# Kernel optimization log

Hardware: AMD Instinct MI355X
Metric: run time of the kernel (lower is better)

The kernel has to match this reference:

```python
import jax, jax.numpy as jnp
import numpy as np

C = 512
GROUPS = 16
EPS = 1e-6


def group_norm(x, gamma, beta):
    # x: (b, c, h, w)
    b, c, h, w = x.shape
    xg = x.reshape(b, GROUPS, c // GROUPS, h, w)
    mean = xg.mean(axis=(2, 3, 4), keepdims=True)
    var = xg.var(axis=(2, 3, 4), keepdims=True)
    xn = ((xg - mean) * jax.lax.rsqrt(var + EPS)).reshape(b, c, h, w)
    return xn * gamma[None, :, None, None] + beta[None, :, None, None]


def setup_inputs() -> dict:
    key = jax.random.key(0)
    ks = jax.random.split(key, 9)
    scale = 1.0 / np.sqrt(C)
    x = jax.random.normal(ks[0], (32, C, 32, 32), dtype=jnp.float32)
    return {
        "x": x,
        "gn_gamma": jnp.ones((C,), jnp.float32),
        "gn_beta": jnp.zeros((C,), jnp.float32),
        "wq": jax.random.normal(ks[1], (C, C), jnp.float32) * scale,
        "bq": jnp.zeros((C,), jnp.float32),
        "wk": jax.random.normal(ks[2], (C, C), jnp.float32) * scale,
        "bk": jnp.zeros((C,), jnp.float32),
        "wv": jax.random.normal(ks[3], (C, C), jnp.float32) * scale,
        "bv": jnp.zeros((C,), jnp.float32),
        "wp": jax.random.normal(ks[4], (C, C), jnp.float32) * scale,
        "bp": jnp.zeros((C,), jnp.float32),
    }


def reference(x, gn_gamma, gn_beta, wq, bq, wk, bk, wv, bv, wp, bp):
    b, c, h, w = x.shape
    hn = group_norm(x, gn_gamma, gn_beta).reshape(b, c, h * w)  # (b, c, n)
    # 1x1 convs == per-token channel GEMMs
    q = jnp.einsum('oc,bcn->bon', wq, hn) + bq[None, :, None]
    k = jnp.einsum('oc,bcn->bon', wk, hn) + bk[None, :, None]
    v = jnp.einsum('oc,bcn->bon', wv, hn) + bv[None, :, None]
    # scores: (b, n, m) = q^T k, scaled
    s = jnp.einsum('bcn,bcm->bnm', q, k) * (float(c) ** -0.5)
    # original subtracts the global max (shift-invariant) then softmax over dim 2
    s = s - jnp.max(s)
    attn = jax.nn.softmax(s, axis=2)
    # h_ = v @ attn^T  -> (b, c, n)
    out = jnp.einsum('bcm,bnm->bcn', v, attn)
    out = jnp.einsum('oc,bcn->bon', wp, out) + bp[None, :, None]
    return x + out.reshape(b, c, h, w)
```

## Files before the change

kernel.cpp:

```cpp
#include <hip/hip_runtime.h>
#include <hip/hip_bf16.h>

typedef unsigned short u16;
typedef __attribute__((ext_vector_type(8))) short bf16x8;
typedef __attribute__((ext_vector_type(4))) float f32x4;

__device__ __forceinline__ u16 f2bf(float f) {
  union { float f; unsigned u; } a; a.f = f;
  unsigned r = a.u + 0x7fffu + ((a.u >> 16) & 1u);
  return (u16)(r >> 16);
}

__device__ __forceinline__ u16 f2h(float f) {
  union { _Float16 h; u16 u; } c; c.h = (_Float16)f; return c.u;
}

__device__ __forceinline__ void stage_ht(const u16* __restrict__ g, int ldg,
                                         u16* __restrict__ s, int tid) {
  int lane = tid & 63, wave = tid >> 6;
#pragma unroll
  for (int t = 0; t < 2; ++t) {
    int cbase = t * 512 + wave * 64;
    int c = cbase + lane;
    int row = c >> 3;
    int q = (c & 7) ^ (row & 7);
    __builtin_amdgcn_global_load_lds(
        (const __attribute__((address_space(1))) unsigned int*)(g + (long)row * ldg + (q << 3)),
        (__attribute__((address_space(3))) unsigned int*)(s + cbase * 8),
        16, 0, 0);
  }
}

__device__ __forceinline__ void ld_a(const u16* __restrict__ Ah, int mh,
                                     int lrow, int quad, int sw, bf16x8 (&a)[4][2]) {
#pragma unroll
  for (int i = 0; i < 4; ++i) {
    int rb = (mh * 64 + i * 16 + lrow) * 64;
#pragma unroll
    for (int ks = 0; ks < 2; ++ks)
      a[i][ks] = *(const bf16x8*)&Ah[rb + (((ks * 4 + quad) ^ sw) << 3)];
  }
}

__device__ __forceinline__ void ld_b(const u16* __restrict__ Bh, int wn1, int nh,
                                     int lrow, int quad, int sw, bf16x8 (&bq)[2][2]) {
#pragma unroll
  for (int j = 0; j < 2; ++j) {
    int rb = (wn1 * 64 + (nh * 2 + j) * 16 + lrow) * 64;
#pragma unroll
    for (int ks = 0; ks < 2; ++ks)
      bq[j][ks] = *(const bf16x8*)&Bh[rb + (((ks * 4 + quad) ^ sw) << 3)];
  }
}

template <int MH, int NH>
__device__ __forceinline__ void mfma_q(bf16x8 (&a)[4][2], bf16x8 (&bq)[2][2],
                                       f32x4 (&acc)[8][4]) {
#pragma unroll
  for (int i = 0; i < 4; ++i)
#pragma unroll
    for (int j = 0; j < 2; ++j) {
      f32x4 c = acc[MH * 4 + i][NH * 2 + j];
      c = __builtin_amdgcn_mfma_f32_16x16x32_bf16(a[i][0], bq[j][0], c, 0, 0, 0);
      c = __builtin_amdgcn_mfma_f32_16x16x32_bf16(a[i][1], bq[j][1], c, 0, 0, 0);
      acc[MH * 4 + i][NH * 2 + j] = c;
    }
}

__device__ __forceinline__ void gemm256_core(
    const u16* __restrict__ Ab, const u16* __restrict__ Bb,
    int lda, int ldb, int K, int tid,
    u16* __restrict__ As, u16* __restrict__ Bs, f32x4 (&acc)[8][4]) {
  int wave = tid >> 6, lane = tid & 63;
  int wm = wave >> 2, wn = wave & 3, wn1 = wn & 1;
  int lrow = lane & 15, quad = lane >> 4;
  int sw = lrow & 7;
#pragma unroll
  for (int i = 0; i < 8; ++i)
#pragma unroll
    for (int j = 0; j < 4; ++j) acc[i][j] = (f32x4){0.f, 0.f, 0.f, 0.f};
  int nkt = K >> 6;
  stage_ht(Ab, lda, As, tid);
  stage_ht(Ab + 128L * lda, lda, As + 8192, tid);
  stage_ht(Bb, ldb, Bs, tid);
  stage_ht(Bb + 128L * ldb, ldb, Bs + 8192, tid);
  for (int kt = 0; kt < nkt; ++kt) {
    __syncthreads();
    const u16* Ah = As + ((kt & 1) * 2 + wm) * 8192;
    const u16* Bh = Bs + ((kt & 1) * 2 + (wn >> 1)) * 8192;
    bf16x8 a0[4][2], a1[4][2], bq0[2][2], bq1[2][2];
    ld_a(Ah, 0, lrow, quad, sw, a0);
    ld_b(Bh, wn1, 0, lrow, quad, sw, bq0);
    if (kt + 1 < nkt) {
      long ko = (long)(kt + 1) * 64;
      int nb = ((kt & 1) ^ 1) * 2;
      stage_ht(Ab + ko, lda, As + nb * 8192, tid);
      stage_ht(Ab + 128L * lda + ko, lda, As + (nb + 1) * 8192, tid);
      stage_ht(Bb + ko, ldb, Bs + nb * 8192, tid);
      stage_ht(Bb + 128L * ldb + ko, ldb, Bs + (nb + 1) * 8192, tid);
    }
    ld_b(Bh, wn1, 1, lrow, quad, sw, bq1);
    ld_a(Ah, 1, lrow, quad, sw, a1);
    __builtin_amdgcn_s_setprio(1);
    mfma_q<0, 0>(a0, bq0, acc);
    mfma_q<0, 1>(a0, bq1, acc);
    mfma_q<1, 1>(a1, bq1, acc);
    mfma_q<1, 0>(a1, bq0, acc);
    __builtin_amdgcn_s_setprio(0);
  }
}

__device__ __forceinline__ void epi_trans_bf16(
    f32x4 (&acc)[8][4], u16* __restrict__ C, long cbase, int m0, int n0, int ldc,
    const float* __restrict__ bias, float scale, int wm, int wn, int lrow, int quad) {
#pragma unroll
  for (int mf = 0; mf < 8; ++mf) {
    int rowbase = m0 + wm * 128 + mf * 16 + quad * 4;
    float4 b4 = bias ? *(const float4*)&bias[rowbase] : make_float4(0.f, 0.f, 0.f, 0.f);
#pragma unroll
    for (int nf = 0; nf < 4; ++nf) {
      int col = n0 + wn * 64 + nf * 16 + lrow;
      f32x4 a = acc[mf][nf];
      uint2 o;
      o.x = (unsigned)f2bf(a[0] * scale + b4.x) | ((unsigned)f2bf(a[1] * scale + b4.y) << 16);
      o.y = (unsigned)f2bf(a[2] * scale + b4.z) | ((unsigned)f2bf(a[3] * scale + b4.w) << 16);
      *(uint2*)(C + cbase + (long)col * ldc + rowbase) = o;
    }
  }
}

template <int MODE>
__global__ __launch_bounds__(512, 2) void gemm_kernel(
    const u16* __restrict__ Ag, const u16* __restrict__ Bg,
    void* __restrict__ C0, void* __restrict__ C1, void* __restrict__ C2,
    const float* __restrict__ bias0, const float* __restrict__ bias1,
    const float* __restrict__ bias2, const float* __restrict__ resid,
    int lda, int ldb, int ldc,
    long strideA, long strideB, long strideC, int K, float scale) {
  extern __shared__ u16 smem[];
  u16* As = smem;
  u16* Bs = smem + 32768;
  int tid = threadIdx.x;
  int b = blockIdx.z;
  int m0 = blockIdx.y * 256, n0 = blockIdx.x * 256;
  const u16* Ab = Ag + (long)b * strideA + (long)m0 * lda;
  const u16* Bb = Bg + (long)b * strideB + (long)n0 * ldb;
  f32x4 acc[8][4];
  gemm256_core(Ab, Bb, lda, ldb, K, tid, As, Bs, acc);

  int wave = tid >> 6, lane = tid & 63;
  int wm = wave >> 2, wn = wave & 3;
  int lrow = lane & 15, quad = lane >> 4;
  long cbase = (long)b * strideC;

  if (MODE == 0) {
    epi_trans_bf16(acc, (u16*)C0, cbase, m0, n0, ldc, bias0, scale, wm, wn, lrow, quad);
  } else if (MODE == 1) {
#pragma unroll
    for (int mf = 0; mf < 8; ++mf)
#pragma unroll
      for (int r = 0; r < 4; ++r) {
        int row = m0 + wm * 128 + mf * 16 + quad * 4 + r;
#pragma unroll
        for (int nf = 0; nf < 4; ++nf) {
          int col = n0 + wn * 64 + nf * 16 + lrow;
          ((u16*)C0)[cbase + (long)row * ldc + col] = f2h(acc[mf][nf][r] * scale);
        }
      }
  } else if (MODE == 2) {
#pragma unroll
    for (int mf = 0; mf < 8; ++mf)
#pragma unroll
      for (int r = 0; r < 4; ++r) {
        int row = m0 + wm * 128 + mf * 16 + quad * 4 + r;
        float bv = bias0[row];
#pragma unroll
        for (int nf = 0; nf < 4; ++nf) {
          int col = n0 + wn * 64 + nf * 16 + lrow;
          long idx = cbase + (long)row * ldc + col;
          ((float*)C0)[idx] = acc[mf][nf][r] * scale + bv + resid[idx];
        }
      }
  } else {
    int seg = m0 >> 9;
    int ml = m0 & 511;
    if (seg == 0) {
      epi_trans_bf16(acc, (u16*)C0, cbase, ml, n0, 512, bias0, 1.f, wm, wn, lrow, quad);
    } else if (seg == 1) {
      epi_trans_bf16(acc, (u16*)C1, cbase, ml, n0, 512, bias1, 1.f, wm, wn, lrow, quad);
    } else {
#pragma unroll
      for (int mf = 0; mf < 8; ++mf)
#pragma unroll
        for (int r = 0; r < 4; ++r) {
          int row = ml + wm * 128 + mf * 16 + quad * 4 + r;
          float bv = bias2[row];
#pragma unroll
          for (int nf = 0; nf < 4; ++nf) {
            int col = n0 + wn * 64 + nf * 16 + lrow;
            ((u16*)C2)[cbase + (long)row * 1024 + col] = f2bf(acc[mf][nf][r] + bv);
          }
        }
    }
  }
}

__global__ __launch_bounds__(256) void groupnorm_kernel(
    const float* __restrict__ x, const float* __restrict__ gamma,
    const float* __restrict__ beta, u16* __restrict__ hnT) {
  int g = blockIdx.x, b = blockIdx.y;
  const float* xb = x + ((long)b * 512 + g * 32) * 1024;
  int tid = threadIdx.x;
  float s = 0.f, sq = 0.f;
  float4 vals[32];
#pragma unroll
  for (int j = 0; j < 32; ++j) {
    float4 v = *(const float4*)(xb + (long)j * 1024 + tid * 4);
    vals[j] = v;
    s += v.x + v.y + v.z + v.w;
    sq += v.x * v.x + v.y * v.y + v.z * v.z + v.w * v.w;
  }
#pragma unroll
  for (int off = 1; off < 64; off <<= 1) {
    s += __shfl_xor(s, off);
    sq += __shfl_xor(sq, off);
  }
  __shared__ float ls[4], lq[4];
  if ((tid & 63) == 0) { ls[tid >> 6] = s; lq[tid >> 6] = sq; }
  __syncthreads();
  float ts = ls[0] + ls[1] + ls[2] + ls[3];
  float tq = lq[0] + lq[1] + lq[2] + lq[3];
  float mean = ts * (1.f / 32768.f);
  float var = tq * (1.f / 32768.f) - mean * mean;
  float rstd = rsqrtf(var + 1e-6f);
  u16* hb = hnT + (long)b * (1024 * 512) + g * 32;
#pragma unroll
  for (int t = 0; t < 4; ++t) {
    u16 row[32];
#pragma unroll
    for (int j = 0; j < 32; ++j) {
      float xv = ((const float*)&vals[j])[t];
      row[j] = f2bf((xv - mean) * rstd * gamma[g * 32 + j] + beta[g * 32 + j]);
    }
    uint4* dst = (uint4*)(hb + (long)(tid * 4 + t) * 512);
    const uint4* src = (const uint4*)row;
    dst[0] = src[0]; dst[1] = src[1]; dst[2] = src[2]; dst[3] = src[3];
  }
}

__global__ __launch_bounds__(256) void softmax_kernel(u16* __restrict__ s) {
  long row = blockIdx.x;
  u16* sr = s + row * 1024;
  int tid = threadIdx.x;
  union { uint2 u; _Float16 h[4]; } c;
  c.u = *(const uint2*)(sr + tid * 4);
  float v0 = (float)c.h[0], v1 = (float)c.h[1], v2 = (float)c.h[2], v3 = (float)c.h[3];
  float m = fmaxf(fmaxf(v0, v1), fmaxf(v2, v3));
#pragma unroll
  for (int off = 1; off < 64; off <<= 1) m = fmaxf(m, __shfl_xor(m, off));
  __shared__ float lm[4], lsum[4];
  if ((tid & 63) == 0) lm[tid >> 6] = m;
  __syncthreads();
  float rowmax = fmaxf(fmaxf(lm[0], lm[1]), fmaxf(lm[2], lm[3]));
  float e0 = expf(v0 - rowmax), e1 = expf(v1 - rowmax);
  float e2 = expf(v2 - rowmax), e3 = expf(v3 - rowmax);
  float sum = e0 + e1 + e2 + e3;
#pragma unroll
  for (int off = 1; off < 64; off <<= 1) sum += __shfl_xor(sum, off);
  if ((tid & 63) == 0) lsum[tid >> 6] = sum;
  __syncthreads();
  float inv = 1.f / (lsum[0] + lsum[1] + lsum[2] + lsum[3]);
  uint2 o;
  o.x = (unsigned)f2bf(e0 * inv) | ((unsigned)f2bf(e1 * inv) << 16);
  o.y = (unsigned)f2bf(e2 * inv) | ((unsigned)f2bf(e3 * inv) << 16);
  *(uint2*)(sr + tid * 4) = o;
}

__global__ __launch_bounds__(256) void convertw_kernel(
    const float* __restrict__ w0, const float* __restrict__ w1,
    const float* __restrict__ w2, const float* __restrict__ w3,
    u16* __restrict__ out) {
  int wsel = blockIdx.x >> 8;
  const float* src = wsel == 0 ? w0 : wsel == 1 ? w1 : wsel == 2 ? w2 : w3;
  int idx = ((blockIdx.x & 255) * 256 + threadIdx.x) * 4;
  float4 v = *(const float4*)(src + idx);
  uint2 o;
  o.x = (unsigned)f2bf(v.x) | ((unsigned)f2bf(v.y) << 16);
  o.y = (unsigned)f2bf(v.z) | ((unsigned)f2bf(v.w) << 16);
  *(uint2*)(out + (long)wsel * 262144 + idx) = o;
}

extern "C" void kernel_launch(void* const* d_in, const int* in_sizes, int n_in,
                              void* d_out, int out_size, void* d_ws, size_t ws_size,
                              hipStream_t stream) {
  const float* x     = (const float*)d_in[0];
  const float* gamma = (const float*)d_in[1];
  const float* beta  = (const float*)d_in[2];
  const float* wq    = (const float*)d_in[3];
  const float* bq    = (const float*)d_in[4];
  const float* wk    = (const float*)d_in[5];
  const float* bk    = (const float*)d_in[6];
  const float* wv    = (const float*)d_in[7];
  const float* bv    = (const float*)d_in[8];
  const float* wp    = (const float*)d_in[9];
  const float* bp    = (const float*)d_in[10];
  float* out = (float*)d_out;
  char* ws = (char*)d_ws;

  static int attr_done = 0;
  if (!attr_done) {
    hipFuncSetAttribute((const void*)gemm_kernel<0>, hipFuncAttributeMaxDynamicSharedMemorySize, 131072);
    hipFuncSetAttribute((const void*)gemm_kernel<1>, hipFuncAttributeMaxDynamicSharedMemorySize, 131072);
    hipFuncSetAttribute((const void*)gemm_kernel<2>, hipFuncAttributeMaxDynamicSharedMemorySize, 131072);
    hipFuncSetAttribute((const void*)gemm_kernel<3>, hipFuncAttributeMaxDynamicSharedMemorySize, 131072);
    attr_done = 1;
  }

  u16* wbf = (u16*)ws;
  u16* hnT = (u16*)(ws + (2L << 20));
  u16* qT  = (u16*)(ws + (34L << 20));
  u16* kT  = (u16*)(ws + (66L << 20));
  u16* v   = (u16*)(ws + (98L << 20));
  u16* s16 = (u16*)(ws + (130L << 20));
  u16* aoT = hnT;

  const long SB = 512L * 1024;
  const long SS = 1024L * 1024;
  const float scale = 0.044194173824159216f;

  convertw_kernel<<<1024, 256, 0, stream>>>(wq, wk, wv, wp, wbf);
  groupnorm_kernel<<<dim3(16, 32), 256, 0, stream>>>(x, gamma, beta, hnT);

  gemm_kernel<3><<<dim3(4, 6, 32), 512, 131072, stream>>>(
      wbf, hnT, qT, kT, v, bq, bk, bv, nullptr,
      512, 512, 0, 0, SB, SB, 512, 1.f);

  gemm_kernel<1><<<dim3(4, 4, 32), 512, 131072, stream>>>(
      qT, kT, s16, nullptr, nullptr, nullptr, nullptr, nullptr, nullptr,
      512, 512, 1024, SB, SB, SS, 512, scale);

  softmax_kernel<<<32 * 1024, 256, 0, stream>>>(s16);

  gemm_kernel<0><<<dim3(4, 2, 32), 512, 131072, stream>>>(
      v, s16, aoT, nullptr, nullptr, nullptr, nullptr, nullptr, nullptr,
      1024, 1024, 512, SB, SS, SB, 1024, 1.f);

  gemm_kernel<2><<<dim3(4, 2, 32), 512, 131072, stream>>>(
      wbf + 3 * 262144, aoT, out, nullptr, nullptr, bp, nullptr, nullptr, x,
      512, 512, 1024, 0, SB, SB, 512, 1.f);
}
```

Before: 362.5 us.

## Use 1024-thread GEMM blocks with 16 waves each owning a 64x64 tile

The 256x256 GEMM tile goes from 8 waves (each 128x64) to 16 waves (each 64x64), so every thread holds half as many accumulators. The staging routine now issues one async global-to-LDS load per thread instead of two. The aim is more waves in flight to hide LDS and global latency. The cost is more LDS fragment reads per MFMA and heavier barrier synchronisation, and __launch_bounds__(1024,4) may force register spills; with 128KB of LDS per block, only one block fits per CU anyway.

```diff
diff --git a/kernel.cpp b/kernel.cpp
--- a/kernel.cpp
+++ b/kernel.cpp
@@ -17,66 +17,24 @@
 
 __device__ __forceinline__ void stage_ht(const u16* __restrict__ g, int ldg,
                                          u16* __restrict__ s, int tid) {
-  int lane = tid & 63, wave = tid >> 6;
-#pragma unroll
-  for (int t = 0; t < 2; ++t) {
-    int cbase = t * 512 + wave * 64;
-    int c = cbase + lane;
-    int row = c >> 3;
-    int q = (c & 7) ^ (row & 7);
-    __builtin_amdgcn_global_load_lds(
-        (const __attribute__((address_space(1))) unsigned int*)(g + (long)row * ldg + (q << 3)),
-        (__attribute__((address_space(3))) unsigned int*)(s + cbase * 8),
-        16, 0, 0);
-  }
-}
-
-__device__ __forceinline__ void ld_a(const u16* __restrict__ Ah, int mh,
-                                     int lrow, int quad, int sw, bf16x8 (&a)[4][2]) {
-#pragma unroll
-  for (int i = 0; i < 4; ++i) {
-    int rb = (mh * 64 + i * 16 + lrow) * 64;
-#pragma unroll
-    for (int ks = 0; ks < 2; ++ks)
-      a[i][ks] = *(const bf16x8*)&Ah[rb + (((ks * 4 + quad) ^ sw) << 3)];
-  }
-}
-
-__device__ __forceinline__ void ld_b(const u16* __restrict__ Bh, int wn1, int nh,
-                                     int lrow, int quad, int sw, bf16x8 (&bq)[2][2]) {
-#pragma unroll
-  for (int j = 0; j < 2; ++j) {
-    int rb = (wn1 * 64 + (nh * 2 + j) * 16 + lrow) * 64;
-#pragma unroll
-    for (int ks = 0; ks < 2; ++ks)
-      bq[j][ks] = *(const bf16x8*)&Bh[rb + (((ks * 4 + quad) ^ sw) << 3)];
-  }
-}
-
-template <int MH, int NH>
-__device__ __forceinline__ void mfma_q(bf16x8 (&a)[4][2], bf16x8 (&bq)[2][2],
-                                       f32x4 (&acc)[8][4]) {
-#pragma unroll
-  for (int i = 0; i < 4; ++i)
-#pragma unroll
-    for (int j = 0; j < 2; ++j) {
-      f32x4 c = acc[MH * 4 + i][NH * 2 + j];
-      c = __builtin_amdgcn_mfma_f32_16x16x32_bf16(a[i][0], bq[j][0], c, 0, 0, 0);
-      c = __builtin_amdgcn_mfma_f32_16x16x32_bf16(a[i][1], bq[j][1], c, 0, 0, 0);
-      acc[MH * 4 + i][NH * 2 + j] = c;
-    }
+  int row = tid >> 3;
+  int q = (tid & 7) ^ (row & 7);
+  __builtin_amdgcn_global_load_lds(
+      (const __attribute__((address_space(1))) unsigned int*)(g + (long)row * ldg + (q << 3)),
+      (__attribute__((address_space(3))) unsigned int*)(s + (tid & ~63) * 8),
+      16, 0, 0);
 }
 
 __device__ __forceinline__ void gemm256_core(
     const u16* __restrict__ Ab, const u16* __restrict__ Bb,
     int lda, int ldb, int K, int tid,
-    u16* __restrict__ As, u16* __restrict__ Bs, f32x4 (&acc)[8][4]) {
+    u16* __restrict__ As, u16* __restrict__ Bs, f32x4 (&acc)[4][4]) {
   int wave = tid >> 6, lane = tid & 63;
-  int wm = wave >> 2, wn = wave & 3, wn1 = wn & 1;
+  int wm = wave >> 2, wn = wave & 3;
   int lrow = lane & 15, quad = lane >> 4;
   int sw = lrow & 7;
 #pragma unroll
-  for (int i = 0; i < 8; ++i)
+  for (int i = 0; i < 4; ++i)
 #pragma unroll
     for (int j = 0; j < 4; ++j) acc[i][j] = (f32x4){0.f, 0.f, 0.f, 0.f};
   int nkt = K >> 6;
@@ -86,36 +44,50 @@
   stage_ht(Bb + 128L * ldb, ldb, Bs + 8192, tid);
   for (int kt = 0; kt < nkt; ++kt) {
     __syncthreads();
-    const u16* Ah = As + ((kt & 1) * 2 + wm) * 8192;
-    const u16* Bh = Bs + ((kt & 1) * 2 + (wn >> 1)) * 8192;
-    bf16x8 a0[4][2], a1[4][2], bq0[2][2], bq1[2][2];
-    ld_a(Ah, 0, lrow, quad, sw, a0);
-    ld_b(Bh, wn1, 0, lrow, quad, sw, bq0);
+    const u16* Ah = As + (kt & 1) * 16384;
+    const u16* Bh = Bs + (kt & 1) * 16384;
+    bf16x8 a0[4], b0[4], a1[4], b1[4];
+#pragma unroll
+    for (int i = 0; i < 4; ++i)
+      a0[i] = *(const bf16x8*)&Ah[(wm * 64 + i * 16 + lrow) * 64 + ((quad ^ sw) << 3)];
+#pragma unroll
+    for (int j = 0; j < 4; ++j)
+      b0[j] = *(const bf16x8*)&Bh[(wn * 64 + j * 16 + lrow) * 64 + ((quad ^ sw) << 3)];
     if (kt + 1 < nkt) {
       long ko = (long)(kt + 1) * 64;
-      int nb = ((kt & 1) ^ 1) * 2;
-      stage_ht(Ab + ko, lda, As + nb * 8192, tid);
-      stage_ht(Ab + 128L * lda + ko, lda, As + (nb + 1) * 8192, tid);
-      stage_ht(Bb + ko, ldb, Bs + nb * 8192, tid);
-      stage_ht(Bb + 128L * ldb + ko, ldb, Bs + (nb + 1) * 8192, tid);
+      int nb = ((kt & 1) ^ 1) * 16384;
+      stage_ht(Ab + ko, lda, As + nb, tid);
+      stage_ht(Ab + 128L * lda + ko, lda, As + nb + 8192, tid);
+      stage_ht(Bb + ko, ldb, Bs + nb, tid);
+      stage_ht(Bb + 128L * ldb + ko, ldb, Bs + nb + 8192, tid);
     }
-    ld_b(Bh, wn1, 1, lrow, quad, sw, bq1);
-    ld_a(Ah, 1, lrow, quad, sw, a1);
+#pragma unroll
+    for (int i = 0; i < 4; ++i)
+      a1[i] = *(const bf16x8*)&Ah[(wm * 64 + i * 16 + lrow) * 64 + (((4 + quad) ^ sw) << 3)];
+#pragma unroll
+    for (int j = 0; j < 4; ++j)
+      b1[j] = *(const bf16x8*)&Bh[(wn * 64 + j * 16 + lrow) * 64 + (((4 + quad) ^ sw) << 3)];
     __builtin_amdgcn_s_setprio(1);
-    mfma_q<0, 0>(a0, bq0, acc);
-    mfma_q<0, 1>(a0, bq1, acc);
-    mfma_q<1, 1>(a1, bq1, acc);
-    mfma_q<1, 0>(a1, bq0, acc);
+#pragma unroll
+    for (int j = 0; j < 4; ++j)
+#pragma unroll
+      for (int i = 0; i < 4; ++i)
+        acc[i][j] = __builtin_amdgcn_mfma_f32_16x16x32_bf16(a0[i], b0[j], acc[i][j], 0, 0, 0);
+#pragma unroll
+    for (int j = 0; j < 4; ++j)
+#pragma unroll
+      for (int i = 0; i < 4; ++i)
+        acc[i][j] = __builtin_amdgcn_mfma_f32_16x16x32_bf16(a1[i], b1[j], acc[i][j], 0, 0, 0);
     __builtin_amdgcn_s_setprio(0);
   }
 }
 
 __device__ __forceinline__ void epi_trans_bf16(
-    f32x4 (&acc)[8][4], u16* __restrict__ C, long cbase, int m0, int n0, int ldc,
+    f32x4 (&acc)[4][4], u16* __restrict__ C, long cbase, int m0, int n0, int ldc,
     const float* __restrict__ bias, float scale, int wm, int wn, int lrow, int quad) {
 #pragma unroll
-  for (int mf = 0; mf < 8; ++mf) {
-    int rowbase = m0 + wm * 128 + mf * 16 + quad * 4;
+  for (int mf = 0; mf < 4; ++mf) {
+    int rowbase = m0 + wm * 64 + mf * 16 + quad * 4;
     float4 b4 = bias ? *(const float4*)&bias[rowbase] : make_float4(0.f, 0.f, 0.f, 0.f);
 #pragma unroll
     for (int nf = 0; nf < 4; ++nf) {
@@ -130,7 +102,7 @@
 }
 
 template <int MODE>
-__global__ __launch_bounds__(512, 2) void gemm_kernel(
+__global__ __launch_bounds__(1024, 4) void gemm_kernel(
     const u16* __restrict__ Ag, const u16* __restrict__ Bg,
     void* __restrict__ C0, void* __restrict__ C1, void* __restrict__ C2,
     const float* __restrict__ bias0, const float* __restrict__ bias1,
@@ -145,7 +117,7 @@
   int m0 = blockIdx.y * 256, n0 = blockIdx.x * 256;
   const u16* Ab = Ag + (long)b * strideA + (long)m0 * lda;
   const u16* Bb = Bg + (long)b * strideB + (long)n0 * ldb;
-  f32x4 acc[8][4];
+  f32x4 acc[4][4];
   gemm256_core(Ab, Bb, lda, ldb, K, tid, As, Bs, acc);
 
   int wave = tid >> 6, lane = tid & 63;
@@ -157,10 +129,10 @@
     epi_trans_bf16(acc, (u16*)C0, cbase, m0, n0, ldc, bias0, scale, wm, wn, lrow, quad);
   } else if (MODE == 1) {
 #pragma unroll
-    for (int mf = 0; mf < 8; ++mf)
+    for (int mf = 0; mf < 4; ++mf)
 #pragma unroll
       for (int r = 0; r < 4; ++r) {
-        int row = m0 + wm * 128 + mf * 16 + quad * 4 + r;
+        int row = m0 + wm * 64 + mf * 16 + quad * 4 + r;
 #pragma unroll
         for (int nf = 0; nf < 4; ++nf) {
           int col = n0 + wn * 64 + nf * 16 + lrow;
@@ -169,10 +141,10 @@
       }
   } else if (MODE == 2) {
 #pragma unroll
-    for (int mf = 0; mf < 8; ++mf)
+    for (int mf = 0; mf < 4; ++mf)
 #pragma unroll
       for (int r = 0; r < 4; ++r) {
-        int row = m0 + wm * 128 + mf * 16 + quad * 4 + r;
+        int row = m0 + wm * 64 + mf * 16 + quad * 4 + r;
         float bv = bias0[row];
 #pragma unroll
         for (int nf = 0; nf < 4; ++nf) {
@@ -190,10 +162,10 @@
       epi_trans_bf16(acc, (u16*)C1, cbase, ml, n0, 512, bias1, 1.f, wm, wn, lrow, quad);
     } else {
 #pragma unroll
-      for (int mf = 0; mf < 8; ++mf)
+      for (int mf = 0; mf < 4; ++mf)
 #pragma unroll
         for (int r = 0; r < 4; ++r) {
-          int row = ml + wm * 128 + mf * 16 + quad * 4 + r;
+          int row = ml + wm * 64 + mf * 16 + quad * 4 + r;
           float bv = bias2[row];
 #pragma unroll
           for (int nf = 0; nf < 4; ++nf) {
@@ -331,21 +303,21 @@
   convertw_kernel<<<1024, 256, 0, stream>>>(wq, wk, wv, wp, wbf);
   groupnorm_kernel<<<dim3(16, 32), 256, 0, stream>>>(x, gamma, beta, hnT);
 
-  gemm_kernel<3><<<dim3(4, 6, 32), 512, 131072, stream>>>(
+  gemm_kernel<3><<<dim3(4, 6, 32), 1024, 131072, stream>>>(
       wbf, hnT, qT, kT, v, bq, bk, bv, nullptr,
       512, 512, 0, 0, SB, SB, 512, 1.f);
 
-  gemm_kernel<1><<<dim3(4, 4, 32), 512, 131072, stream>>>(
+  gemm_kernel<1><<<dim3(4, 4, 32), 1024, 131072, stream>>>(
       qT, kT, s16, nullptr, nullptr, nullptr, nullptr, nullptr, nullptr,
       512, 512, 1024, SB, SB, SS, 512, scale);
 
   softmax_kernel<<<32 * 1024, 256, 0, stream>>>(s16);
 
-  gemm_kernel<0><<<dim3(4, 2, 32), 512, 131072, stream>>>(
+  gemm_kernel<0><<<dim3(4, 2, 32), 1024, 131072, stream>>>(
       v, s16, aoT, nullptr, nullptr, nullptr, nullptr, nullptr, nullptr,
       1024, 1024, 512, SB, SS, SB, 1024, 1.f);
 
-  gemm_kernel<2><<<dim3(4, 2, 32), 512, 131072, stream>>>(
+  gemm_kernel<2><<<dim3(4, 2, 32), 1024, 131072, stream>>>(
       wbf + 3 * 262144, aoT, out, nullptr, nullptr, bp, nullptr, nullptr, x,
       512, 512, 1024, 0, SB, SB, 512, 1.f);
 }
```

Result: slower. 659.0 us (+81.8%).
